# Kernel optimization log

Measured on AMD Instinct MI355X. Metric: run time of the kernel, lower is better.

Reference implementation:

```python
import jax, jax.numpy as jnp
import numpy as np

B, N, D_IN, H, NH = 8, 1024, 3072, 128, 4
DH = H // NH
LN_EPS = 1e-5


def make_mask(key, p):
    A = jax.random.bernoulli(key, p, (N, N)).astype(jnp.float32)
    A_tilde = A + jnp.eye(N, dtype=jnp.float32)  # add self-loops
    return jnp.where(A_tilde > 0, 0.0, -jnp.inf).astype(jnp.float32)


def setup_inputs() -> dict:
    key = jax.random.key(0)
    ks = jax.random.split(key, 20)
    s = 0.02
    inp = {
        "stim_features": jax.random.normal(ks[0], (B, D_IN), jnp.float32),
        # stim encoder
        "W_enc1": jax.random.normal(ks[1], (2 * H, D_IN), jnp.float32) * s,
        "b_enc1": jnp.zeros((2 * H,), jnp.float32),
        "ln_g": jnp.ones((2 * H,), jnp.float32),
        "ln_b": jnp.zeros((2 * H,), jnp.float32),
        "W_enc2": jax.random.normal(ks[2], (H, 2 * H), jnp.float32) * s,
        "b_enc2": jnp.zeros((H,), jnp.float32),
        "voxel_emb": jax.random.normal(ks[3], (N, H), jnp.float32) * 0.01,
        # GAT projection weights (Linear, no bias), [out, in]
        "W_func1": jax.random.normal(ks[4], (H, H), jnp.float32) * s,
        "W_roi1": jax.random.normal(ks[5], (H, H), jnp.float32) * s,
        "W_func2": jax.random.normal(ks[6], (H, H), jnp.float32) * s,
        "W_roi2": jax.random.normal(ks[7], (H, H), jnp.float32) * s,
        # fusion / skip / readout
        "W_fu1": jax.random.normal(ks[8], (H, 2 * H), jnp.float32) * s,
        "b_fu1": jnp.zeros((H,), jnp.float32),
        "W_fu2": jax.random.normal(ks[9], (H, 2 * H), jnp.float32) * s,
        "b_fu2": jnp.zeros((H,), jnp.float32),
        "W_sk1": jax.random.normal(ks[10], (H, H), jnp.float32) * s,
        "b_sk1": jnp.zeros((H,), jnp.float32),
        "W_sk2": jax.random.normal(ks[11], (H, H), jnp.float32) * s,
        "b_sk2": jnp.zeros((H,), jnp.float32),
        "W_ro": jax.random.normal(ks[12], (1, H), jnp.float32) * s,
        "b_ro": jnp.zeros((1,), jnp.float32),
        # static adjacency masks (buffers, 0 / -inf)
        "mask_func": make_mask(ks[13], 0.01),
        "mask_roi": make_mask(ks[14], 0.05),
    }
    return inp


def gat(h, W, mask):
    # h: [B, N, H]; W: [H, H]; mask: [N, N]
    Bq, Nq, _ = h.shape
    Wh = (h @ W.T).reshape(Bq, Nq, NH, DH).transpose(0, 2, 1, 3)  # [B, nh, N, dh]
    scores = jnp.einsum("bhnd,bhmd->bhnm", Wh, Wh) / np.sqrt(DH)
    scores = scores + mask[None, None]
    attn = jax.nn.softmax(scores, axis=-1)  # dropout = identity (eval mode)
    hp = jnp.einsum("bhnm,bhmd->bhnd", attn, Wh)
    hp = hp.transpose(0, 2, 1, 3).reshape(Bq, Nq, NH * DH)
    return jax.nn.elu(hp)


def reference(stim_features, W_enc1, b_enc1, ln_g, ln_b, W_enc2, b_enc2,
              voxel_emb, W_func1, W_roi1, W_func2, W_roi2,
              W_fu1, b_fu1, W_fu2, b_fu2, W_sk1, b_sk1, W_sk2, b_sk2,
              W_ro, b_ro, mask_func, mask_roi):
    # stim encoder: Linear -> LayerNorm -> GELU -> Linear (dropout = identity)
    z = stim_features @ W_enc1.T + b_enc1
    mu = jnp.mean(z, axis=-1, keepdims=True)
    var = jnp.var(z, axis=-1, keepdims=True)
    z = (z - mu) * jax.lax.rsqrt(var + LN_EPS) * ln_g + ln_b
    z = jax.nn.gelu(z, approximate=False)
    g = z @ W_enc2.T + b_enc2  # [B, H]

    x = g[:, None, :] + voxel_emb[None]  # [B, N, H]
    x_res1 = x
    h1 = jnp.concatenate([gat(x, W_func1, mask_func), gat(x, W_roi1, mask_roi)], axis=-1)
    x = h1 @ W_fu1.T + b_fu1
    x = x + (x_res1 @ W_sk1.T + b_sk1)
    x_res2 = x
    h2 = jnp.concatenate([gat(x, W_func2, mask_func), gat(x, W_roi2, mask_roi)], axis=-1)
    x = h2 @ W_fu2.T + b_fu2
    x = x + (x_res2 @ W_sk2.T + b_sk2)
    pred = (x @ W_ro.T + b_ro)[..., 0]  # [B, N]
    return pred
```

## Files before the change

### kernel.cpp

```cpp
#include <hip/hip_runtime.h>
#include <hip/hip_bf16.h>
#include <math.h>

#define B_SZ 8
#define N_SZ 1024
#define D_IN 3072
#define H_SZ 128
#define NH 4
#define DH 32
#define TWO_H 256
#define LN_EPS 1e-5f
#define CAP 128

typedef __attribute__((ext_vector_type(8))) short bf16x8;
typedef __attribute__((ext_vector_type(8))) unsigned short u16x8;
typedef __attribute__((ext_vector_type(4))) float f32x4;
typedef __attribute__((ext_vector_type(4))) unsigned int u32x4;

__device__ inline unsigned short f2bf(float f) {
    unsigned int u = __builtin_bit_cast(unsigned int, f);
    u += 0x7fffu + ((u >> 16) & 1u);
    return (unsigned short)(u >> 16);
}

__global__ __launch_bounds__(256) void prep_kernel(
        const float* __restrict__ Wfu1, const float* __restrict__ Wsk1,
        const float* __restrict__ Wfu2, const float* __restrict__ Wsk2,
        const float* __restrict__ Wf1, const float* __restrict__ Wr1,
        const float* __restrict__ Wf2, const float* __restrict__ Wr2,
        unsigned short* __restrict__ wb,
        const float* __restrict__ m0, const float* __restrict__ m1,
        int* __restrict__ i0, int* __restrict__ i1,
        int* __restrict__ d0, int* __restrict__ d1,
        const float* __restrict__ stim, const float* __restrict__ W1,
        const float* __restrict__ b1, float* __restrict__ z) {
    const int bid = blockIdx.x;
    const int tid = threadIdx.x;

    if (bid < 128) {
        const int j = bid;
        wb[j * 384 + tid] = f2bf(Wfu1[j * 256 + tid]);
        wb[49152 + j * 384 + tid] = f2bf(Wfu2[j * 256 + tid]);
        if (tid < 128) {
            wb[j * 384 + 256 + tid]         = f2bf(Wsk1[j * 128 + tid]);
            wb[49152 + j * 384 + 256 + tid] = f2bf(Wsk2[j * 128 + tid]);
            wb[98304  + j * 128 + tid] = f2bf(Wf1[j * 128 + tid]);
            wb[114688 + j * 128 + tid] = f2bf(Wr1[j * 128 + tid]);
            wb[131072 + j * 128 + tid] = f2bf(Wf2[j * 128 + tid]);
            wb[147456 + j * 128 + tid] = f2bf(Wr2[j * 128 + tid]);
        }
    } else if (bid < 640) {
        const int bIdx = bid - 128;
        const int gsel = bIdx >> 8;
        const float* mask = gsel ? m1 : m0;
        int* idx = gsel ? i1 : i0;
        int* deg = gsel ? d1 : d0;
        const int row = (bIdx & 255) * 4 + (tid >> 6);
        const int lane = tid & 63;
        const float* mrow = mask + (size_t)row * N_SZ;
        int* irow = idx + (size_t)row * CAP;

        int base = 0;
        #pragma unroll 4
        for (int t = 0; t < N_SZ / 64; ++t) {
            int c = t * 64 + lane;
            bool edge = (mrow[c] == 0.0f);
            unsigned long long ball = __ballot(edge);
            unsigned long long below = ball & ((1ull << lane) - 1ull);
            if (edge) {
                int p = base + __popcll(below);
                if (p < CAP) irow[p] = c;
            }
            base += __popcll(ball);
        }
        if (lane == 0) deg[row] = (base < CAP) ? base : CAP;
    } else {
        const int j = bid - 640;
        const float4* w4 = (const float4*)(W1 + (size_t)j * D_IN);
        const float4* s4 = (const float4*)stim;

        float acc[B_SZ];
        #pragma unroll
        for (int b = 0; b < B_SZ; ++b) acc[b] = 0.0f;

        #pragma unroll
        for (int i = 0; i < D_IN / 4 / 256; ++i) {
            const int k4 = tid + i * 256;
            const float4 w = w4[k4];
            #pragma unroll
            for (int b = 0; b < B_SZ; ++b) {
                const float4 s = s4[b * (D_IN / 4) + k4];
                acc[b] += s.x * w.x + s.y * w.y + s.z * w.z + s.w * w.w;
            }
        }
        #pragma unroll
        for (int b = 0; b < B_SZ; ++b) {
            float v = acc[b];
            v += __shfl_xor(v, 1);  v += __shfl_xor(v, 2);  v += __shfl_xor(v, 4);
            v += __shfl_xor(v, 8);  v += __shfl_xor(v, 16); v += __shfl_xor(v, 32);
            acc[b] = v;
        }
        __shared__ float red[4][B_SZ];
        const int wave = tid >> 6, lane = tid & 63;
        if (lane == 0) {
            #pragma unroll
            for (int b = 0; b < B_SZ; ++b) red[wave][b] = acc[b];
        }
        __syncthreads();
        if (tid < B_SZ) {
            float v = red[0][tid] + red[1][tid] + red[2][tid] + red[3][tid];
            z[tid * TWO_H + j] = v + b1[j];
        }
    }
}

__global__ __launch_bounds__(256) void enc23_kernel(
        const float* __restrict__ z,
        const float* __restrict__ lng, const float* __restrict__ lnb,
        const float* __restrict__ W2, const float* __restrict__ b2,
        float* __restrict__ g) {
    __shared__ float red[TWO_H];
    __shared__ float zgs[TWO_H];
    __shared__ float gp[2][H_SZ];
    const int b = blockIdx.x;
    const int tid = threadIdx.x;

    float zi = z[b * TWO_H + tid];
    red[tid] = zi; __syncthreads();
    for (int s = 128; s > 0; s >>= 1) { if (tid < s) red[tid] += red[tid + s]; __syncthreads(); }
    float mu = red[0] * (1.0f / TWO_H);
    __syncthreads();
    float dz = zi - mu;
    red[tid] = dz * dz; __syncthreads();
    for (int s = 128; s > 0; s >>= 1) { if (tid < s) red[tid] += red[tid + s]; __syncthreads(); }
    float var = red[0] * (1.0f / TWO_H);

    float zn = dz * (1.0f / sqrtf(var + LN_EPS)) * lng[tid] + lnb[tid];
    zgs[tid] = 0.5f * zn * (1.0f + erff(zn * 0.70710678118654752f));
    __syncthreads();

    const int j = tid & 127, half = tid >> 7;
    const float* w2r = W2 + (size_t)j * TWO_H + half * 128;
    const float* zh = &zgs[half * 128];
    float s = 0.0f;
    #pragma unroll 4
    for (int k = 0; k < 128; ++k) s += zh[k] * w2r[k];
    gp[half][j] = s;
    __syncthreads();
    if (tid < H_SZ) g[b * H_SZ + tid] = gp[0][tid] + gp[1][tid] + b2[tid];
}

template<int NSEG, bool OB16, bool AEMB, bool RO>
__global__ __launch_bounds__(256) void gemm_mfma(
        const float* __restrict__ a0, const float* __restrict__ a1,
        const float* __restrict__ a2,
        const float* __restrict__ gvec, const float* __restrict__ emb,
        const unsigned short* __restrict__ wba, const unsigned short* __restrict__ wbb,
        const float* __restrict__ bias1, const float* __restrict__ bias2,
        float* __restrict__ outa, float* __restrict__ outb,
        const float* __restrict__ Wro, const float* __restrict__ bro,
        float* __restrict__ pred) {
    const unsigned short* wb = blockIdx.y ? wbb : wba;
    float* out = blockIdx.y ? outb : outa;
    const int KW = NSEG * 128;

    __shared__ __align__(16) short As[32 * 128];
    __shared__ __align__(16) short Bs[64 * 128];
    __shared__ float part[2][32];

    const int bid = blockIdx.x;
    const int ct = bid & 1, rt = bid >> 1;
    const int row0 = rt * 32, col0 = ct * 64;
    const int tid = threadIdx.x;
    const int lane = tid & 63, w = tid >> 6;
    const int wm = w >> 1, wn = w & 1;
    const int lrow = lane & 15, lk = lane >> 4;

    f32x4 acc0 = {0.f, 0.f, 0.f, 0.f};
    f32x4 acc1 = {0.f, 0.f, 0.f, 0.f};

    for (int seg = 0; seg < NSEG; ++seg) {
        const float* src = (seg == 0) ? a0 : ((seg == 1) ? a1 : a2);
        const bool useEmb = AEMB && (NSEG == 1 || seg == 2);
        if (seg) __syncthreads();
        for (int gi = tid; gi < 512; gi += 256) {
            const int r = gi >> 4, kq = gi & 15;
            float4 v0, v1;
            if (useEmb) {
                const int row = row0 + r;
                const float4* gp = (const float4*)(gvec + (size_t)(row >> 10) * H_SZ) + kq * 2;
                const float4* ep = (const float4*)(emb + (size_t)(row & 1023) * H_SZ) + kq * 2;
                const float4 g0 = gp[0], g1 = gp[1], e0 = ep[0], e1 = ep[1];
                v0.x = g0.x + e0.x; v0.y = g0.y + e0.y; v0.z = g0.z + e0.z; v0.w = g0.w + e0.w;
                v1.x = g1.x + e1.x; v1.y = g1.y + e1.y; v1.z = g1.z + e1.z; v1.w = g1.w + e1.w;
            } else {
                const float4* sp = (const float4*)(src + (size_t)(row0 + r) * H_SZ) + kq * 2;
                v0 = sp[0]; v1 = sp[1];
            }
            u16x8 t;
            t[0] = f2bf(v0.x); t[1] = f2bf(v0.y); t[2] = f2bf(v0.z); t[3] = f2bf(v0.w);
            t[4] = f2bf(v1.x); t[5] = f2bf(v1.y); t[6] = f2bf(v1.z); t[7] = f2bf(v1.w);
            *(u16x8*)&As[r * 128 + ((kq * 8) ^ ((r & 7) << 3))] = t;
        }
        for (int gi = tid; gi < 1024; gi += 256) {
            const int c = gi >> 4, kq = gi & 15;
            const float4 v = *(const float4*)(wb + (size_t)(col0 + c) * KW + seg * 128 + kq * 8);
            *(float4*)&Bs[c * 128 + ((kq * 8) ^ ((c & 7) << 3))] = v;
        }
        __syncthreads();

        #pragma unroll
        for (int ks = 0; ks < 4; ++ks) {
            const int kof = ks * 32 + lk * 8;
            const int r = wm * 16 + lrow;
            const bf16x8 a = *(const bf16x8*)&As[r * 128 + (kof ^ ((r & 7) << 3))];
            const int c0 = wn * 32 + lrow;
            const bf16x8 b0 = *(const bf16x8*)&Bs[c0 * 128 + (kof ^ ((c0 & 7) << 3))];
            const int c1 = c0 + 16;
            const bf16x8 b1 = *(const bf16x8*)&Bs[c1 * 128 + (kof ^ ((c1 & 7) << 3))];
            acc0 = __builtin_amdgcn_mfma_f32_16x16x32_bf16(a, b0, acc0, 0, 0, 0);
            acc1 = __builtin_amdgcn_mfma_f32_16x16x32_bf16(a, b1, acc1, 0, 0, 0);
        }
    }

    const int rb = row0 + wm * 16 + lk * 4;
    if constexpr (RO) {
        float pr[4] = {0.f, 0.f, 0.f, 0.f};
        #pragma unroll
        for (int fc = 0; fc < 2; ++fc) {
            const int c = col0 + wn * 32 + fc * 16 + lrow;
            const float bias = bias1[c] + bias2[c];
            const float wro = Wro[c];
            const f32x4 a = fc ? acc1 : acc0;
            #pragma unroll
            for (int rr = 0; rr < 4; ++rr) pr[rr] += (a[rr] + bias) * wro;
        }
        #pragma unroll
        for (int rr = 0; rr < 4; ++rr) {
            pr[rr] += __shfl_xor(pr[rr], 1);
            pr[rr] += __shfl_xor(pr[rr], 2);
            pr[rr] += __shfl_xor(pr[rr], 4);
            pr[rr] += __shfl_xor(pr[rr], 8);
        }
        if (lrow == 0) {
            #pragma unroll
            for (int rr = 0; rr < 4; ++rr) part[wn][wm * 16 + lk * 4 + rr] = pr[rr];
        }
        __syncthreads();
        if (tid < 32) {
            float v = part[0][tid] + part[1][tid];
            if (ct == 0) v += bro[0];
            atomicAdd(pred + row0 + tid, v);
        }
    } else {
        #pragma unroll
        for (int fc = 0; fc < 2; ++fc) {
            const int c = col0 + wn * 32 + fc * 16 + lrow;
            const float bias = (bias1 ? bias1[c] : 0.0f) + (bias2 ? bias2[c] : 0.0f);
            const f32x4 a = fc ? acc1 : acc0;
            #pragma unroll
            for (int rr = 0; rr < 4; ++rr) {
                if constexpr (OB16) {
                    ((unsigned short*)out)[(size_t)(rb + rr) * H_SZ + c] = f2bf(a[rr] + bias);
                } else {
                    out[(size_t)(rb + rr) * H_SZ + c] = a[rr] + bias;
                }
            }
        }
    }
}

__global__ __launch_bounds__(256) void attn_kernel(
        const unsigned short* __restrict__ Wha, const unsigned short* __restrict__ Whb,
        const int* __restrict__ ia, const int* __restrict__ ib,
        const int* __restrict__ da, const int* __restrict__ db,
        float* __restrict__ oa, float* __restrict__ ob) {
    const unsigned short* Wh = blockIdx.y ? Whb : Wha;
    const int* idx = blockIdx.y ? ib : ia;
    const int* deg = blockIdx.y ? db : da;
    float* out = blockIdx.y ? ob : oa;

    const int bid = blockIdx.x;
    const int b = bid & 7;
    const int i = ((bid >> 3) << 2) | (threadIdx.x >> 6);
    const int bi = b * N_SZ + i;
    const int lane = threadIdx.x & 63;
    const int c = lane & 15;
    const int e4 = lane >> 4;

    const u32x4 qb = *(const u32x4*)(Wh + (size_t)bi * H_SZ + c * 8);
    float qf[8];
    #pragma unroll
    for (int m = 0; m < 4; ++m) {
        qf[2 * m]     = __builtin_bit_cast(float, qb[m] << 16) * 0.25505654741110714f;
        qf[2 * m + 1] = __builtin_bit_cast(float, qb[m] & 0xffff0000u) * 0.25505654741110714f;
    }

    const int dg = deg[i];
    const int* row = idx + (size_t)i * CAP;
    int idxv0 = row[lane] & 1023;
    int idxv1 = (dg > 64) ? (row[64 + lane] & 1023) : 0;

    const unsigned short* kbase = Wh + (size_t)b * N_SZ * H_SZ;

    float acc[8];
    #pragma unroll
    for (int k = 0; k < 8; ++k) acc[k] = 0.0f;
    float l = 0.0f;

    const int nseg = (dg + 15) >> 4;
    for (int seg = 0; seg < nseg; ++seg) {
        const int srcv = (seg >= 4) ? idxv1 : idxv0;
        const int off16 = (seg & 3) << 4;
        u32x4 kv[4];
        #pragma unroll
        for (int t = 0; t < 4; ++t) {
            const int j0 = __builtin_amdgcn_readlane(srcv, off16 + 4 * t);
            const int j1 = __builtin_amdgcn_readlane(srcv, off16 + 4 * t + 1);
            const int j2 = __builtin_amdgcn_readlane(srcv, off16 + 4 * t + 2);
            const int j3 = __builtin_amdgcn_readlane(srcv, off16 + 4 * t + 3);
            const int jlo = (e4 & 1) ? j1 : j0;
            const int jhi = (e4 & 1) ? j3 : j2;
            const int j = (e4 & 2) ? jhi : jlo;
            kv[t] = *(const u32x4*)(kbase + (size_t)j * H_SZ + c * 8);
        }
        const int ebase = seg << 4;
        #pragma unroll
        for (int t = 0; t < 4; ++t) {
            float kf[8];
            #pragma unroll
            for (int m = 0; m < 4; ++m) {
                kf[2 * m]     = __builtin_bit_cast(float, kv[t][m] << 16);
                kf[2 * m + 1] = __builtin_bit_cast(float, kv[t][m] & 0xffff0000u);
            }
            float s = 0.0f;
            #pragma unroll
            for (int k = 0; k < 8; ++k) s += qf[k] * kf[k];
            s += __shfl_xor(s, 1);
            s += __shfl_xor(s, 2);
            const bool valid = (ebase + 4 * t + e4) < dg;
            const float p = valid ? __builtin_amdgcn_exp2f(s) : 0.0f;
            l += p;
            #pragma unroll
            for (int k = 0; k < 8; ++k) acc[k] += p * kf[k];
        }
    }

    l += __shfl_xor(l, 16);
    l += __shfl_xor(l, 32);
    #pragma unroll
    for (int k = 0; k < 8; ++k) {
        acc[k] += __shfl_xor(acc[k], 16);
        acc[k] += __shfl_xor(acc[k], 32);
    }

    if (e4 == 0) {
        const float inv = 1.0f / l;
        float o[8];
        #pragma unroll
        for (int k = 0; k < 8; ++k) {
            const float hp = acc[k] * inv;
            o[k] = (hp > 0.0f) ? hp
                 : (__builtin_amdgcn_exp2f(hp * 1.4426950408889634f) - 1.0f);
        }
        float4 v0 = {o[0], o[1], o[2], o[3]};
        float4 v1 = {o[4], o[5], o[6], o[7]};
        *(float4*)(out + (size_t)bi * H_SZ + c * 8) = v0;
        *(float4*)(out + (size_t)bi * H_SZ + c * 8 + 4) = v1;
    }
}

extern "C" void kernel_launch(void* const* d_in, const int* in_sizes, int n_in,
                              void* d_out, int out_size, void* d_ws, size_t ws_size,
                              hipStream_t stream) {
    const float* stim   = (const float*)d_in[0];
    const float* W_enc1 = (const float*)d_in[1];
    const float* b_enc1 = (const float*)d_in[2];
    const float* ln_g   = (const float*)d_in[3];
    const float* ln_b   = (const float*)d_in[4];
    const float* W_enc2 = (const float*)d_in[5];
    const float* b_enc2 = (const float*)d_in[6];
    const float* vox    = (const float*)d_in[7];
    const float* W_f1   = (const float*)d_in[8];
    const float* W_r1   = (const float*)d_in[9];
    const float* W_f2   = (const float*)d_in[10];
    const float* W_r2   = (const float*)d_in[11];
    const float* W_fu1  = (const float*)d_in[12];
    const float* b_fu1  = (const float*)d_in[13];
    const float* W_fu2  = (const float*)d_in[14];
    const float* b_fu2  = (const float*)d_in[15];
    const float* W_sk1  = (const float*)d_in[16];
    const float* b_sk1  = (const float*)d_in[17];
    const float* W_sk2  = (const float*)d_in[18];
    const float* b_sk2  = (const float*)d_in[19];
    const float* W_ro   = (const float*)d_in[20];
    const float* b_ro   = (const float*)d_in[21];
    const float* mask_f = (const float*)d_in[22];
    const float* mask_r = (const float*)d_in[23];

    float* pred = (float*)d_out;

    float* ws  = (float*)d_ws;
    float* z   = ws;
    float* g   = z + 2048;
    float* x2  = g + 1024;
    float* hf  = x2 + 1048576;
    float* hr  = hf + 1048576;
    unsigned short* Whf16 = (unsigned short*)(hr + 1048576);
    unsigned short* Whr16 = Whf16 + 1048576;
    int* idxf  = (int*)(Whr16 + 1048576);
    int* idxr  = idxf + N_SZ * CAP;
    int* degf  = idxr + N_SZ * CAP;
    int* degr  = degf + N_SZ;
    unsigned short* wb16 = (unsigned short*)(degr + N_SZ);
    unsigned short* wcat1 = wb16;
    unsigned short* wcat2 = wb16 + 49152;
    unsigned short* wpf1  = wb16 + 98304;
    unsigned short* wpr1  = wb16 + 114688;
    unsigned short* wpf2  = wb16 + 131072;
    unsigned short* wpr2  = wb16 + 147456;

    const int BN = B_SZ * N_SZ;

    hipMemsetAsync(pred, 0, BN * sizeof(float), stream);

    prep_kernel<<<896, 256, 0, stream>>>(
        W_fu1, W_sk1, W_fu2, W_sk2, W_f1, W_r1, W_f2, W_r2, wb16,
        mask_f, mask_r, idxf, idxr, degf, degr,
        stim, W_enc1, b_enc1, z);
    enc23_kernel<<<B_SZ, 256, 0, stream>>>(z, ln_g, ln_b, W_enc2, b_enc2, g);

    gemm_mfma<1, true, true, false><<<dim3(BN / 32 * 2, 2), 256, 0, stream>>>(
        nullptr, nullptr, nullptr, g, vox, wpf1, wpr1, nullptr, nullptr,
        (float*)Whf16, (float*)Whr16, nullptr, nullptr, nullptr);
    attn_kernel<<<dim3(BN / 4, 2), 256, 0, stream>>>(Whf16, Whr16, idxf, idxr, degf, degr,
                                                     hf, hr);
    gemm_mfma<3, false, true, false><<<dim3(BN / 32 * 2, 1), 256, 0, stream>>>(
        hf, hr, nullptr, g, vox, wcat1, wcat1, b_fu1, b_sk1,
        x2, x2, nullptr, nullptr, nullptr);

    gemm_mfma<1, true, false, false><<<dim3(BN / 32 * 2, 2), 256, 0, stream>>>(
        x2, nullptr, nullptr, nullptr, nullptr, wpf2, wpr2, nullptr, nullptr,
        (float*)Whf16, (float*)Whr16, nullptr, nullptr, nullptr);
    attn_kernel<<<dim3(BN / 4, 2), 256, 0, stream>>>(Whf16, Whr16, idxf, idxr, degf, degr,
                                                     hf, hr);
    gemm_mfma<3, false, false, true><<<dim3(BN / 32 * 2, 1), 256, 0, stream>>>(
        hf, hr, x2, nullptr, nullptr, wcat2, wcat2, b_fu2, b_sk2,
        nullptr, nullptr, W_ro, b_ro, pred);
}
```

Before: 100.7 us.

## Store intermediate activations in bf16 and software-pipeline attention gather loads

Attention outputs (hf, hr) and the fused layer-1 output x2 are now written and read as bf16 instead of fp32, and the GEMM gains a bf16 A-input path that skips the fp32-to-bf16 conversion. This halves the memory traffic for these intermediates. The attention kernel also double-buffers its neighbour key gathers so the next segment's loads are issued before the current segment is computed. The cost is extra rounding of the residual x2 and of the attention outputs, plus higher register pressure in the attention kernel.

```diff
diff --git a/kernel.cpp b/kernel.cpp
--- a/kernel.cpp
+++ b/kernel.cpp
@@ -150,18 +150,18 @@
     if (tid < H_SZ) g[b * H_SZ + tid] = gp[0][tid] + gp[1][tid] + b2[tid];
 }
 
-template<int NSEG, bool OB16, bool AEMB, bool RO>
+template<int NSEG, bool OB16, bool AEMB, bool RO, bool AB16>
 __global__ __launch_bounds__(256) void gemm_mfma(
-        const float* __restrict__ a0, const float* __restrict__ a1,
-        const float* __restrict__ a2,
+        const void* __restrict__ a0, const void* __restrict__ a1,
+        const void* __restrict__ a2,
         const float* __restrict__ gvec, const float* __restrict__ emb,
         const unsigned short* __restrict__ wba, const unsigned short* __restrict__ wbb,
         const float* __restrict__ bias1, const float* __restrict__ bias2,
-        float* __restrict__ outa, float* __restrict__ outb,
+        void* __restrict__ outa, void* __restrict__ outb,
         const float* __restrict__ Wro, const float* __restrict__ bro,
         float* __restrict__ pred) {
     const unsigned short* wb = blockIdx.y ? wbb : wba;
-    float* out = blockIdx.y ? outb : outa;
+    void* out = blockIdx.y ? outb : outa;
     const int KW = NSEG * 128;
 
     __shared__ __align__(16) short As[32 * 128];
@@ -180,26 +180,31 @@
     f32x4 acc1 = {0.f, 0.f, 0.f, 0.f};
 
     for (int seg = 0; seg < NSEG; ++seg) {
-        const float* src = (seg == 0) ? a0 : ((seg == 1) ? a1 : a2);
+        const void* src = (seg == 0) ? a0 : ((seg == 1) ? a1 : a2);
         const bool useEmb = AEMB && (NSEG == 1 || seg == 2);
         if (seg) __syncthreads();
         for (int gi = tid; gi < 512; gi += 256) {
             const int r = gi >> 4, kq = gi & 15;
-            float4 v0, v1;
+            u16x8 t;
             if (useEmb) {
                 const int row = row0 + r;
                 const float4* gp = (const float4*)(gvec + (size_t)(row >> 10) * H_SZ) + kq * 2;
                 const float4* ep = (const float4*)(emb + (size_t)(row & 1023) * H_SZ) + kq * 2;
                 const float4 g0 = gp[0], g1 = gp[1], e0 = ep[0], e1 = ep[1];
-                v0.x = g0.x + e0.x; v0.y = g0.y + e0.y; v0.z = g0.z + e0.z; v0.w = g0.w + e0.w;
-                v1.x = g1.x + e1.x; v1.y = g1.y + e1.y; v1.z = g1.z + e1.z; v1.w = g1.w + e1.w;
+                t[0] = f2bf(g0.x + e0.x); t[1] = f2bf(g0.y + e0.y);
+                t[2] = f2bf(g0.z + e0.z); t[3] = f2bf(g0.w + e0.w);
+                t[4] = f2bf(g1.x + e1.x); t[5] = f2bf(g1.y + e1.y);
+                t[6] = f2bf(g1.z + e1.z); t[7] = f2bf(g1.w + e1.w);
+            } else if (AB16) {
+                t = *(const u16x8*)((const unsigned short*)src
+                                    + (size_t)(row0 + r) * H_SZ + kq * 8);
             } else {
-                const float4* sp = (const float4*)(src + (size_t)(row0 + r) * H_SZ) + kq * 2;
-                v0 = sp[0]; v1 = sp[1];
+                const float4* sp = (const float4*)((const float*)src
+                                    + (size_t)(row0 + r) * H_SZ) + kq * 2;
+                const float4 v0 = sp[0], v1 = sp[1];
+                t[0] = f2bf(v0.x); t[1] = f2bf(v0.y); t[2] = f2bf(v0.z); t[3] = f2bf(v0.w);
+                t[4] = f2bf(v1.x); t[5] = f2bf(v1.y); t[6] = f2bf(v1.z); t[7] = f2bf(v1.w);
             }
-            u16x8 t;
-            t[0] = f2bf(v0.x); t[1] = f2bf(v0.y); t[2] = f2bf(v0.z); t[3] = f2bf(v0.w);
-            t[4] = f2bf(v1.x); t[5] = f2bf(v1.y); t[6] = f2bf(v1.z); t[7] = f2bf(v1.w);
             *(u16x8*)&As[r * 128 + ((kq * 8) ^ ((r & 7) << 3))] = t;
         }
         for (int gi = tid; gi < 1024; gi += 256) {
@@ -263,7 +268,7 @@
                 if constexpr (OB16) {
                     ((unsigned short*)out)[(size_t)(rb + rr) * H_SZ + c] = f2bf(a[rr] + bias);
                 } else {
-                    out[(size_t)(rb + rr) * H_SZ + c] = a[rr] + bias;
+                    ((float*)out)[(size_t)(rb + rr) * H_SZ + c] = a[rr] + bias;
                 }
             }
         }
@@ -274,11 +279,11 @@
         const unsigned short* __restrict__ Wha, const unsigned short* __restrict__ Whb,
         const int* __restrict__ ia, const int* __restrict__ ib,
         const int* __restrict__ da, const int* __restrict__ db,
-        float* __restrict__ oa, float* __restrict__ ob) {
+        unsigned short* __restrict__ oa, unsigned short* __restrict__ ob) {
     const unsigned short* Wh = blockIdx.y ? Whb : Wha;
     const int* idx = blockIdx.y ? ib : ia;
     const int* deg = blockIdx.y ? db : da;
-    float* out = blockIdx.y ? ob : oa;
+    unsigned short* out = blockIdx.y ? ob : oa;
 
     const int bid = blockIdx.x;
     const int b = bid & 7;
@@ -308,11 +313,9 @@
     for (int k = 0; k < 8; ++k) acc[k] = 0.0f;
     float l = 0.0f;
 
-    const int nseg = (dg + 15) >> 4;
-    for (int seg = 0; seg < nseg; ++seg) {
-        const int srcv = (seg >= 4) ? idxv1 : idxv0;
-        const int off16 = (seg & 3) << 4;
-        u32x4 kv[4];
+    auto loadSeg = [&](int s, u32x4* kv) {
+        const int srcv = (s >= 4) ? idxv1 : idxv0;
+        const int off16 = (s & 3) << 4;
         #pragma unroll
         for (int t = 0; t < 4; ++t) {
             const int j0 = __builtin_amdgcn_readlane(srcv, off16 + 4 * t);
@@ -324,7 +327,9 @@
             const int j = (e4 & 2) ? jhi : jlo;
             kv[t] = *(const u32x4*)(kbase + (size_t)j * H_SZ + c * 8);
         }
-        const int ebase = seg << 4;
+    };
+    auto computeSeg = [&](int s, const u32x4* kv) {
+        const int ebase = s << 4;
         #pragma unroll
         for (int t = 0; t < 4; ++t) {
             float kf[8];
@@ -333,17 +338,30 @@
                 kf[2 * m]     = __builtin_bit_cast(float, kv[t][m] << 16);
                 kf[2 * m + 1] = __builtin_bit_cast(float, kv[t][m] & 0xffff0000u);
             }
-            float s = 0.0f;
-            #pragma unroll
-            for (int k = 0; k < 8; ++k) s += qf[k] * kf[k];
-            s += __shfl_xor(s, 1);
-            s += __shfl_xor(s, 2);
+            float s2 = 0.0f;
+            #pragma unroll
+            for (int k = 0; k < 8; ++k) s2 += qf[k] * kf[k];
+            s2 += __shfl_xor(s2, 1);
+            s2 += __shfl_xor(s2, 2);
             const bool valid = (ebase + 4 * t + e4) < dg;
-            const float p = valid ? __builtin_amdgcn_exp2f(s) : 0.0f;
+            const float p = valid ? __builtin_amdgcn_exp2f(s2) : 0.0f;
             l += p;
             #pragma unroll
             for (int k = 0; k < 8; ++k) acc[k] += p * kf[k];
         }
+    };
+
+    const int nseg = (dg + 15) >> 4;
+    u32x4 kvA[4], kvB[4];
+    loadSeg(0, kvA);
+    int seg = 0;
+    while (true) {
+        if (seg + 1 < nseg) loadSeg(seg + 1, kvB);
+        computeSeg(seg, kvA);
+        ++seg; if (seg >= nseg) break;
+        if (seg + 1 < nseg) loadSeg(seg + 1, kvA);
+        computeSeg(seg, kvB);
+        ++seg; if (seg >= nseg) break;
     }
 
     l += __shfl_xor(l, 16);
@@ -356,17 +374,15 @@
 
     if (e4 == 0) {
         const float inv = 1.0f / l;
-        float o[8];
+        u16x8 ov;
         #pragma unroll
         for (int k = 0; k < 8; ++k) {
             const float hp = acc[k] * inv;
-            o[k] = (hp > 0.0f) ? hp
+            const float o = (hp > 0.0f) ? hp
                  : (__builtin_amdgcn_exp2f(hp * 1.4426950408889634f) - 1.0f);
-        }
-        float4 v0 = {o[0], o[1], o[2], o[3]};
-        float4 v1 = {o[4], o[5], o[6], o[7]};
-        *(float4*)(out + (size_t)bi * H_SZ + c * 8) = v0;
-        *(float4*)(out + (size_t)bi * H_SZ + c * 8 + 4) = v1;
+            ov[k] = f2bf(o);
+        }
+        *(u16x8*)(out + (size_t)bi * H_SZ + c * 8) = ov;
     }
 }
 
@@ -403,10 +419,10 @@
     float* ws  = (float*)d_ws;
     float* z   = ws;
     float* g   = z + 2048;
-    float* x2  = g + 1024;
-    float* hf  = x2 + 1048576;
-    float* hr  = hf + 1048576;
-    unsigned short* Whf16 = (unsigned short*)(hr + 1048576);
+    unsigned short* x2_16 = (unsigned short*)(g + 1024);
+    unsigned short* hf16  = x2_16 + 1048576;
+    unsigned short* hr16  = hf16 + 1048576;
+    unsigned short* Whf16 = hr16 + 1048576;
     unsigned short* Whr16 = Whf16 + 1048576;
     int* idxf  = (int*)(Whr16 + 1048576);
     int* idxr  = idxf + N_SZ * CAP;
@@ -430,21 +446,21 @@
         stim, W_enc1, b_enc1, z);
     enc23_kernel<<<B_SZ, 256, 0, stream>>>(z, ln_g, ln_b, W_enc2, b_enc2, g);
 
-    gemm_mfma<1, true, true, false><<<dim3(BN / 32 * 2, 2), 256, 0, stream>>>(
+    gemm_mfma<1, true, true, false, false><<<dim3(BN / 32 * 2, 2), 256, 0, stream>>>(
         nullptr, nullptr, nullptr, g, vox, wpf1, wpr1, nullptr, nullptr,
-        (float*)Whf16, (float*)Whr16, nullptr, nullptr, nullptr);
+        Whf16, Whr16, nullptr, nullptr, nullptr);
     attn_kernel<<<dim3(BN / 4, 2), 256, 0, stream>>>(Whf16, Whr16, idxf, idxr, degf, degr,
-                                                     hf, hr);
-    gemm_mfma<3, false, true, false><<<dim3(BN / 32 * 2, 1), 256, 0, stream>>>(
-        hf, hr, nullptr, g, vox, wcat1, wcat1, b_fu1, b_sk1,
-        x2, x2, nullptr, nullptr, nullptr);
-
-    gemm_mfma<1, true, false, false><<<dim3(BN / 32 * 2, 2), 256, 0, stream>>>(
-        x2, nullptr, nullptr, nullptr, nullptr, wpf2, wpr2, nullptr, nullptr,
-        (float*)Whf16, (float*)Whr16, nullptr, nullptr, nullptr);
+                                                     hf16, hr16);
+    gemm_mfma<3, true, true, false, true><<<dim3(BN / 32 * 2, 1), 256, 0, stream>>>(
+        hf16, hr16, nullptr, g, vox, wcat1, wcat1, b_fu1, b_sk1,
+        x2_16, x2_16, nullptr, nullptr, nullptr);
+
+    gemm_mfma<1, true, false, false, true><<<dim3(BN / 32 * 2, 2), 256, 0, stream>>>(
+        x2_16, nullptr, nullptr, nullptr, nullptr, wpf2, wpr2, nullptr, nullptr,
+        Whf16, Whr16, nullptr, nullptr, nullptr);
     attn_kernel<<<dim3(BN / 4, 2), 256, 0, stream>>>(Whf16, Whr16, idxf, idxr, degf, degr,
-                                                     hf, hr);
-    gemm_mfma<3, false, false, true><<<dim3(BN / 32 * 2, 1), 256, 0, stream>>>(
-        hf, hr, x2, nullptr, nullptr, wcat2, wcat2, b_fu2, b_sk2,
+                                                     hf16, hr16);
+    gemm_mfma<3, false, false, true, true><<<dim3(BN / 32 * 2, 1), 256, 0, stream>>>(
+        hf16, hr16, x2_16, nullptr, nullptr, wcat2, wcat2, b_fu2, b_sk2,
         nullptr, nullptr, W_ro, b_ro, pred);
 }
```

After: 96.76 us. 1.04x faster.
